# Performance work log

Hardware: AMD Instinct MI355X
Metric: run time of the kernel (lower is better)

The kernel has to match this reference:

```python
import jax, jax.numpy as jnp
import numpy as np

B, L, H = 32, 2048, 512


def setup_inputs() -> dict:
    key = jax.random.key(0)
    k1, k2, k3, k4, k5, k6 = jax.random.split(key, 6)
    scale = 1.0 / np.sqrt(H)
    return {
        "query": jax.random.normal(k1, (B, H), dtype=jnp.float32),
        "ref": jax.random.normal(k2, (B, L, H), dtype=jnp.float32),
        "mask": jax.random.randint(k3, (B, L), 0, 2) == 1,
        # learned params (torch Linear weight layout: [out, in]; apply as x @ W.T)
        "W_ref": jax.random.normal(k4, (H, H), dtype=jnp.float32) * scale,
        "W_q": jax.random.normal(k5, (H, H), dtype=jnp.float32) * scale,
        "v": jax.random.normal(k6, (H,), dtype=jnp.float32) * scale,
    }


def reference(query, ref, mask, W_ref, W_q, v):
    scale = 1.0 / np.sqrt(H)
    # additive (Bahdanau) scores: v^T tanh(W_ref ref + W_q q)
    encoded_ref = jnp.einsum("blh,oh->blo", ref, W_ref)          # (B, L, H)
    encoded_q = jnp.einsum("bh,oh->bo", query, W_q)[:, None, :]  # (B, 1, H)
    scores = jnp.einsum("blh,h->bl", jnp.tanh(encoded_ref + encoded_q), v)
    scores = scores * scale
    scores = jnp.where(mask, -1e9, scores)
    attn = jax.nn.softmax(scores, axis=1)                         # (B, L)
    glimpse = jnp.einsum("bl,blh->bh", attn, ref)                 # (B, H)
    return glimpse, scores
```

## Files before the change

kernel.cpp:

```cpp
#include <hip/hip_runtime.h>
#include <hip/hip_bf16.h>
#include <cstdint>

typedef __attribute__((ext_vector_type(4))) float f32x4;
typedef __attribute__((ext_vector_type(8))) short s16x8;

#define NB   32
#define NL   2048
#define NH   512
#define NM   (NB * NL)
#define SCALE 0.04419417382415922f

__device__ __forceinline__ ushort f2bf(float f) {
    __hip_bfloat16 b = __float2bfloat16(f);
    return *reinterpret_cast<ushort*>(&b);
}
__device__ __forceinline__ unsigned long long pack4(float4 f) {
    union { ushort u[4]; unsigned long long v; } p;
    p.u[0] = f2bf(f.x); p.u[1] = f2bf(f.y); p.u[2] = f2bf(f.z); p.u[3] = f2bf(f.w);
    return p.v;
}

__device__ __forceinline__ void gl16(const ushort* g, ushort* l) {
    __builtin_amdgcn_global_load_lds(
        (const __attribute__((address_space(1))) unsigned int*)g,
        (__attribute__((address_space(3))) unsigned int*)l,
        16, 0, 0);
}

__global__ __launch_bounds__(256) void k_pre(const float* __restrict__ W,
                                             ushort* __restrict__ Wb,
                                             const float* __restrict__ query,
                                             const float* __restrict__ Wq,
                                             float* __restrict__ eq) {
    int bid = blockIdx.x;
    int t = threadIdx.x;
    if (bid < 64) {
        const float4* F = (const float4*)W;
        unsigned long long* U = (unsigned long long*)Wb;
        int base = bid * 1024 + t;
        float4 f[4];
#pragma unroll
        for (int k = 0; k < 4; ++k) f[k] = F[base + k * 256];
#pragma unroll
        for (int k = 0; k < 4; ++k) U[base + k * 256] = pack4(f[k]);
    } else {
        __shared__ float q[NH];
        int b = bid - 64;
        q[t] = query[b * NH + t];
        q[t + 256] = query[b * NH + t + 256];
        __syncthreads();
#pragma unroll
        for (int half = 0; half < 2; ++half) {
            int o = t + half * 256;
            const float4* w = (const float4*)(Wq + (size_t)o * NH);
            float acc = 0.f;
#pragma unroll 4
            for (int i = 0; i < NH / 4; ++i) {
                float4 x = w[i];
                acc += q[4 * i] * x.x + q[4 * i + 1] * x.y + q[4 * i + 2] * x.z + q[4 * i + 3] * x.w;
            }
            eq[b * NH + o] = acc;
        }
    }
}

__global__ __launch_bounds__(512, 4) void k_gemm_full(const float* __restrict__ ref,
                                                      const ushort* __restrict__ Wb,
                                                      const float* __restrict__ eq,
                                                      const float* __restrict__ v,
                                                      const int* __restrict__ mask,
                                                      float* __restrict__ out_sc) {
    __shared__ ushort Bs[2][512 * 32];
    __shared__ ushort As[2][64 * 36];
    __shared__ float sc_red[8][64];

    int tid = threadIdx.x;
    int lane = tid & 63, wid = tid >> 6;
    int blk = blockIdx.x;
    int m0g = blk << 6;
    int b = blk >> 5;

    f32x4 acc[4][4];
#pragma unroll
    for (int i = 0; i < 4; ++i)
#pragma unroll
        for (int j = 0; j < 4; ++j) acc[i][j] = (f32x4)(0.f);

    const ushort* bglob = Wb + ((size_t)(wid * 64) + (lane >> 2)) * NH + (lane & 3) * 8;
    int arow = tid >> 3, acol = (tid & 7) * 4;
    const float* aglob = ref + (size_t)(m0g + arow) * NH + acol;
    int awr = arow * 36 + acol;

    int lr = lane & 15, kq = lane >> 4;
    int aof = lr * 36 + kq * 8;
    int bof = (wid * 64 + lr) * 32 + kq * 8;

#define STAGE_B(buf, kt)                                                     \
    {   gl16(bglob + (kt) * 32,               &Bs[buf][(wid * 64) * 32]);    \
        gl16(bglob + (kt) * 32 + 16 * NH,     &Bs[buf][(wid * 64 + 16) * 32]); \
        gl16(bglob + (kt) * 32 + 32 * NH,     &Bs[buf][(wid * 64 + 32) * 32]); \
        gl16(bglob + (kt) * 32 + 48 * NH,     &Bs[buf][(wid * 64 + 48) * 32]); }

#define LOAD_A(kt)   pa = *(const float4*)(aglob + (kt) * 32);

#define WRITE_A(buf) { *(unsigned long long*)&As[buf][awr] = pack4(pa); }

#define READ_FRAGS(buf)                                                      \
    _Pragma("unroll")                                                        \
    for (int f = 0; f < 4; ++f) af[f] = *(const s16x8*)&As[buf][aof + f * 16 * 36]; \
    _Pragma("unroll")                                                        \
    for (int f = 0; f < 4; ++f) bfr[f] = *(const s16x8*)&Bs[buf][bof + f * 16 * 32];

#define DO_MFMA()                                                            \
    _Pragma("unroll")                                                        \
    for (int fr = 0; fr < 4; ++fr)                                           \
        _Pragma("unroll")                                                    \
        for (int fc = 0; fc < 4; ++fc)                                       \
            acc[fr][fc] = __builtin_amdgcn_mfma_f32_16x16x32_bf16(af[fr], bfr[fc], acc[fr][fc], 0, 0, 0);

    float4 pa;
    LOAD_A(0)
    WRITE_A(0)
    STAGE_B(0, 0)
    __syncthreads();

    for (int t2 = 0; t2 < 8; ++t2) {
        s16x8 af[4], bfr[4];
        int k0 = 2 * t2;
        if (k0 + 1 < 16) { LOAD_A(k0 + 1) STAGE_B(1, k0 + 1) }
        READ_FRAGS(0)
        DO_MFMA()
        if (k0 + 1 < 16) WRITE_A(1)
        __syncthreads();
        if (k0 + 2 < 16) { LOAD_A(k0 + 2) STAGE_B(0, k0 + 2) }
        READ_FRAGS(1)
        DO_MFMA()
        if (k0 + 2 < 16) WRITE_A(0)
        __syncthreads();
    }
#undef STAGE_B
#undef LOAD_A
#undef WRITE_A
#undef READ_FRAGS
#undef DO_MFMA

    const float* eqb = eq + b * NH;
    float vv[4], ee[4];
#pragma unroll
    for (int fc = 0; fc < 4; ++fc) {
        int c = wid * 64 + fc * 16 + lr;
        vv[fc] = v[c];
        ee[fc] = eqb[c];
    }
#pragma unroll
    for (int fr = 0; fr < 4; ++fr) {
#pragma unroll
        for (int reg = 0; reg < 4; ++reg) {
            float s = 0.f;
#pragma unroll
            for (int fc = 0; fc < 4; ++fc) {
                float x = acc[fr][fc][reg] + ee[fc];
                float t = 1.f - 2.f / (__expf(2.f * x) + 1.f);
                s += vv[fc] * t;
            }
            s += __shfl_xor(s, 1);
            s += __shfl_xor(s, 2);
            s += __shfl_xor(s, 4);
            s += __shfl_xor(s, 8);
            if (lr == 0) sc_red[wid][fr * 16 + kq * 4 + reg] = s;
        }
    }
    __syncthreads();
    if (tid < 64) {
        float t = 0.f;
#pragma unroll
        for (int w = 0; w < 8; ++w) t += sc_red[w][tid];
        t *= SCALE;
        int rg = m0g + tid;
        if (mask[rg] != 0) t = -1e9f;
        out_sc[rg] = t;
    }
}

__global__ __launch_bounds__(256) void k_smglp(const float* __restrict__ scores,
                                               const float* __restrict__ ref,
                                               float* __restrict__ glp) {
    int sp = blockIdx.x, b = blockIdx.y;
    int tid = threadIdx.x;
    int lane = tid & 63, wid = tid >> 6;
    __shared__ float red[4];
    __shared__ float asl[128];
    float sc[8];
    float mx = -3.4e38f;
#pragma unroll
    for (int i = 0; i < 8; ++i) {
        sc[i] = scores[b * NL + i * 256 + tid];
        mx = fmaxf(mx, sc[i]);
    }
#pragma unroll
    for (int o = 32; o >= 1; o >>= 1) mx = fmaxf(mx, __shfl_xor(mx, o));
    if (lane == 0) red[wid] = mx;
    __syncthreads();
    mx = fmaxf(fmaxf(red[0], red[1]), fmaxf(red[2], red[3]));
    __syncthreads();
    float ls = 0.f;
#pragma unroll
    for (int i = 0; i < 8; ++i) {
        float e = __expf(sc[i] - mx);
        ls += e;
        if (i == (sp >> 1) && (tid >> 7) == (sp & 1)) asl[tid & 127] = e;
    }
#pragma unroll
    for (int o = 32; o >= 1; o >>= 1) ls += __shfl_xor(ls, o);
    if (lane == 0) red[wid] = ls;
    __syncthreads();
    float inv = 1.f / (red[0] + red[1] + red[2] + red[3]);

    const float* rb = ref + ((size_t)b * NL + sp * 128) * NH;
    float2 acc = make_float2(0.f, 0.f);
#pragma unroll 4
    for (int l = 0; l < 128; ++l) {
        float a = asl[l];
        float2 r = ((const float2*)(rb + (size_t)l * NH))[tid];
        acc.x += a * r.x;
        acc.y += a * r.y;
    }
    acc.x *= inv;
    acc.y *= inv;
    ((float2*)(glp + (size_t)(sp * NB + b) * NH))[tid] = acc;
}

__global__ __launch_bounds__(256) void k_gred(const float* __restrict__ glp,
                                              float* __restrict__ out_gl) {
    int idx = blockIdx.x * 256 + threadIdx.x;
    float s = 0.f;
#pragma unroll
    for (int sp = 0; sp < 16; ++sp) s += glp[sp * (NB * NH) + idx];
    out_gl[idx] = s;
}

extern "C" void kernel_launch(void* const* d_in, const int* in_sizes, int n_in,
                              void* d_out, int out_size, void* d_ws, size_t ws_size,
                              hipStream_t stream) {
    const float* query = (const float*)d_in[0];
    const float* ref   = (const float*)d_in[1];
    const int*   mask  = (const int*)d_in[2];
    const float* W_ref = (const float*)d_in[3];
    const float* W_q   = (const float*)d_in[4];
    const float* v     = (const float*)d_in[5];

    float* out_gl = (float*)d_out;
    float* out_sc = out_gl + NB * NH;

    char* w = (char*)d_ws;
    ushort* wW = (ushort*)w;
    float* eq  = (float*)(w + 524288);
    float* glp = (float*)(w + 589824);

    k_pre<<<96, 256, 0, stream>>>(W_ref, wW, query, W_q, eq);
    k_gemm_full<<<1024, 512, 0, stream>>>(ref, wW, eq, v, mask, out_sc);
    k_smglp<<<dim3(16, NB), 256, 0, stream>>>(out_sc, ref, glp);
    k_gred<<<64, 256, 0, stream>>>(glp, out_gl);
}
```

Before: 123.2 us.

## Stage fp32 A tiles directly to LDS and swizzle both operand layouts

The ref (A) operand is now copied from global memory straight into LDS as fp32 with global_load_lds, in place of being loaded into registers, packed to bf16 and written by hand. The fp32-to-bf16 conversion moves to fragment-read time. Both the A and B LDS tiles get an XOR swizzle, which replaces the padding used to avoid bank conflicts. This removes register staging and the LDS write instructions, at the cost of redundant per-wave conversion work, twice the A LDS footprint, and a larger shared buffer that is reused for the score reduction.

```diff
diff --git a/kernel.cpp b/kernel.cpp
--- a/kernel.cpp
+++ b/kernel.cpp
@@ -21,12 +21,10 @@
     return p.v;
 }
 
-__device__ __forceinline__ void gl16(const ushort* g, ushort* l) {
-    __builtin_amdgcn_global_load_lds(
-        (const __attribute__((address_space(1))) unsigned int*)g,
-        (__attribute__((address_space(3))) unsigned int*)l,
-        16, 0, 0);
-}
+#define GL16(g, l)                                                         \
+    __builtin_amdgcn_global_load_lds(                                      \
+        (const __attribute__((address_space(1))) unsigned int*)(g),        \
+        (__attribute__((address_space(3))) unsigned int*)(l), 16, 0, 0)
 
 __global__ __launch_bounds__(256) void k_pre(const float* __restrict__ W,
                                              ushort* __restrict__ Wb,
@@ -71,9 +69,11 @@
                                                       const float* __restrict__ v,
                                                       const int* __restrict__ mask,
                                                       float* __restrict__ out_sc) {
-    __shared__ ushort Bs[2][512 * 32];
-    __shared__ ushort As[2][64 * 36];
-    __shared__ float sc_red[8][64];
+    __shared__ char smem[81920];
+    ushort* Bs0 = (ushort*)smem;
+    ushort* Bs1 = (ushort*)(smem + 32768);
+    float*  As0 = (float*)(smem + 65536);
+    float*  As1 = (float*)(smem + 73728);
 
     int tid = threadIdx.x;
     int lane = tid & 63, wid = tid >> 6;
@@ -87,64 +87,63 @@
 #pragma unroll
         for (int j = 0; j < 4; ++j) acc[i][j] = (f32x4)(0.f);
 
-    const ushort* bglob = Wb + ((size_t)(wid * 64) + (lane >> 2)) * NH + (lane & 3) * 8;
-    int arow = tid >> 3, acol = (tid & 7) * 4;
-    const float* aglob = ref + (size_t)(m0g + arow) * NH + acol;
-    int awr = arow * 36 + acol;
+    const ushort* bglob = Wb + ((size_t)(wid * 64) + (lane >> 2)) * NH
+                             + (((lane & 3) ^ ((lane >> 3) & 3)) << 3);
+    const float* aglob = ref + (size_t)(m0g + wid * 8 + (lane >> 3)) * NH
+                             + (((lane & 7) ^ ((lane >> 3) & 7)) << 2);
 
     int lr = lane & 15, kq = lane >> 4;
-    int aof = lr * 36 + kq * 8;
-    int bof = (wid * 64 + lr) * 32 + kq * 8;
-
-#define STAGE_B(buf, kt)                                                     \
-    {   gl16(bglob + (kt) * 32,               &Bs[buf][(wid * 64) * 32]);    \
-        gl16(bglob + (kt) * 32 + 16 * NH,     &Bs[buf][(wid * 64 + 16) * 32]); \
-        gl16(bglob + (kt) * 32 + 32 * NH,     &Bs[buf][(wid * 64 + 32) * 32]); \
-        gl16(bglob + (kt) * 32 + 48 * NH,     &Bs[buf][(wid * 64 + 48) * 32]); }
-
-#define LOAD_A(kt)   pa = *(const float4*)(aglob + (kt) * 32);
-
-#define WRITE_A(buf) { *(unsigned long long*)&As[buf][awr] = pack4(pa); }
-
-#define READ_FRAGS(buf)                                                      \
-    _Pragma("unroll")                                                        \
-    for (int f = 0; f < 4; ++f) af[f] = *(const s16x8*)&As[buf][aof + f * 16 * 36]; \
-    _Pragma("unroll")                                                        \
-    for (int f = 0; f < 4; ++f) bfr[f] = *(const s16x8*)&Bs[buf][bof + f * 16 * 32];
-
-#define DO_MFMA()                                                            \
-    _Pragma("unroll")                                                        \
-    for (int fr = 0; fr < 4; ++fr)                                           \
-        _Pragma("unroll")                                                    \
-        for (int fc = 0; fc < 4; ++fc)                                       \
-            acc[fr][fc] = __builtin_amdgcn_mfma_f32_16x16x32_bf16(af[fr], bfr[fc], acc[fr][fc], 0, 0, 0);
-
-    float4 pa;
-    LOAD_A(0)
-    WRITE_A(0)
-    STAGE_B(0, 0)
+    int bbase = (wid * 64 + lr) * 32 + ((kq ^ ((lr >> 1) & 3)) << 3);
+    int arow = lr * 32;
+    int ac0 = (((2 * kq) ^ (lr & 7)) << 2);
+    int ac1 = (((2 * kq + 1) ^ (lr & 7)) << 2);
+
+#define STAGE(Bsb, Asb, kt)                                           \
+    {   GL16(bglob + (kt) * 32,            Bsb + (wid * 64) * 32);    \
+        GL16(bglob + (kt) * 32 + 16 * NH,  Bsb + (wid * 64 + 16) * 32); \
+        GL16(bglob + (kt) * 32 + 32 * NH,  Bsb + (wid * 64 + 32) * 32); \
+        GL16(bglob + (kt) * 32 + 48 * NH,  Bsb + (wid * 64 + 48) * 32); \
+        GL16(aglob + (kt) * 32,            Asb + (wid * 8) * 32); }
+
+#define READ_COMPUTE(Bsb, Asb)                                                   \
+    {   s16x8 bfr[4], af[4];                                                     \
+        _Pragma("unroll")                                                        \
+        for (int f = 0; f < 4; ++f) bfr[f] = *(const s16x8*)&Bsb[bbase + f * 512]; \
+        _Pragma("unroll")                                                        \
+        for (int f = 0; f < 4; ++f) {                                            \
+            float4 a0 = *(const float4*)(Asb + arow + f * 512 + ac0);            \
+            float4 a1 = *(const float4*)(Asb + arow + f * 512 + ac1);            \
+            union { ushort u[8]; s16x8 v; } p;                                   \
+            p.u[0] = f2bf(a0.x); p.u[1] = f2bf(a0.y);                            \
+            p.u[2] = f2bf(a0.z); p.u[3] = f2bf(a0.w);                            \
+            p.u[4] = f2bf(a1.x); p.u[5] = f2bf(a1.y);                            \
+            p.u[6] = f2bf(a1.z); p.u[7] = f2bf(a1.w);                            \
+            af[f] = p.v;                                                         \
+        }                                                                        \
+        _Pragma("unroll")                                                        \
+        for (int fr = 0; fr < 4; ++fr)                                           \
+            _Pragma("unroll")                                                    \
+            for (int fc = 0; fc < 4; ++fc)                                       \
+                acc[fr][fc] = __builtin_amdgcn_mfma_f32_16x16x32_bf16(           \
+                    af[fr], bfr[fc], acc[fr][fc], 0, 0, 0);                      \
+    }
+
+    STAGE(Bs0, As0, 0)
     __syncthreads();
 
     for (int t2 = 0; t2 < 8; ++t2) {
-        s16x8 af[4], bfr[4];
         int k0 = 2 * t2;
-        if (k0 + 1 < 16) { LOAD_A(k0 + 1) STAGE_B(1, k0 + 1) }
-        READ_FRAGS(0)
-        DO_MFMA()
-        if (k0 + 1 < 16) WRITE_A(1)
+        STAGE(Bs1, As1, k0 + 1)
+        READ_COMPUTE(Bs0, As0)
         __syncthreads();
-        if (k0 + 2 < 16) { LOAD_A(k0 + 2) STAGE_B(0, k0 + 2) }
-        READ_FRAGS(1)
-        DO_MFMA()
-        if (k0 + 2 < 16) WRITE_A(0)
+        if (k0 + 2 < 16) STAGE(Bs0, As0, k0 + 2)
+        READ_COMPUTE(Bs1, As1)
         __syncthreads();
     }
-#undef STAGE_B
-#undef LOAD_A
-#undef WRITE_A
-#undef READ_FRAGS
-#undef DO_MFMA
-
+#undef STAGE
+#undef READ_COMPUTE
+
+    float* sc_red = (float*)smem;
     const float* eqb = eq + b * NH;
     float vv[4], ee[4];
 #pragma unroll
@@ -168,14 +167,14 @@
             s += __shfl_xor(s, 2);
             s += __shfl_xor(s, 4);
             s += __shfl_xor(s, 8);
-            if (lr == 0) sc_red[wid][fr * 16 + kq * 4 + reg] = s;
+            if (lr == 0) sc_red[wid * 64 + fr * 16 + kq * 4 + reg] = s;
         }
     }
     __syncthreads();
     if (tid < 64) {
         float t = 0.f;
 #pragma unroll
-        for (int w = 0; w < 8; ++w) t += sc_red[w][tid];
+        for (int w = 0; w < 8; ++w) t += sc_red[w * 64 + tid];
         t *= SCALE;
         int rg = m0g + tid;
         if (mask[rg] != 0) t = -1e9f;
```

New measurement: 124.9 us. Within noise of the previous version (+1.4%).
